# Performance work log

Measured on AMD Instinct MI355X. Metric: run time of the kernel, lower is better.

## Reference

```python
import jax, jax.numpy as jnp
import numpy as np

N, D = 768, 64
EPS = 1e-5

def _ln(x, g, b):
    u = x.mean(-1, keepdims=True)
    s = ((x - u) ** 2).mean(-1, keepdims=True)
    return g * (x - u) / jnp.sqrt(s + EPS) + b

def setup_inputs() -> dict:
    key = jax.random.key(0)
    ks = jax.random.split(key, 16)
    inp = {
        'corr_index': jax.random.normal(ks[0], (N, N, 2), dtype=jnp.float32),
        'nei_index': jax.random.randint(ks[1], (N, N), 0, 2, dtype=jnp.int32),
        'nei_num': jax.random.randint(ks[2], (N,), 0, N, dtype=jnp.int32),
        'hidden_state': jax.random.normal(ks[3], (N, D), dtype=jnp.float32),
        'cn': jax.random.normal(ks[4], (N, D), dtype=jnp.float32),
        # relativeLayer: MLP(2 -> D)
        'W_r': jax.random.normal(ks[5], (2, D)) * 0.01, 'b_r': jnp.zeros((D,)),
        'g_r': jnp.ones((D,)), 'be_r': jax.random.normal(ks[6], (D,)) * 0.02,
        # ngate: MLP_gate(3D -> D)
        'W_g': jax.random.normal(ks[7], (3 * D, D)) * 0.01, 'b_g': jnp.zeros((D,)),
        'g_g': jnp.ones((D,)), 'be_g': jax.random.normal(ks[8], (D,)) * 0.02,
        # WAr: MLP(3D -> 1)
        'W_a': jax.random.normal(ks[9], (3 * D, 1)) * 0.01, 'b_a': jnp.zeros((1,)),
        'g_a': jnp.ones((1,)), 'be_a': jnp.abs(jax.random.normal(ks[10], (1,))) * 0.02 + 0.01,
        # weight: MLP(D -> D)
        'W_w': jax.random.normal(ks[11], (D, D)) * 0.01, 'b_w': jnp.zeros((D,)),
        'g_w': jnp.ones((D,)), 'be_w': jax.random.normal(ks[12], (D,)) * 0.02,
    }
    return inp

def reference(corr_index, nei_index, nei_num, hidden_state, cn,
              W_r, b_r, g_r, be_r, W_g, b_g, g_g, be_g,
              W_a, b_a, g_a, be_a, W_w, b_w, g_w, be_w):
    n, d = hidden_state.shape
    mask = nei_index > 0  # [N,N]; (i,j): j is neighbor of i
    # relativeLayer on all pairs (values at masked positions match the torch gather)
    r = jax.nn.relu(_ln(corr_index @ W_r + b_r, g_r, be_r))  # [N,N,D]
    hi = jnp.broadcast_to(hidden_state[:, None, :], (n, n, d))  # hi_t: h[i]
    hj = jnp.broadcast_to(hidden_state[None, :, :], (n, n, d))  # nei_inputs: h[j]
    tmp = jnp.concatenate([r, hi, hj], axis=-1)  # [N,N,3D]
    nGate = jax.nn.sigmoid(_ln(tmp @ W_g + b_g, g_g, be_g))  # [N,N,D]
    tt = jax.nn.relu(_ln(tmp @ W_a + b_a, g_a, be_a))[..., 0]  # [N,N]
    Pos = jnp.where(mask, tt, 0.0)
    Pos = jnp.where(Pos == 0.0, -10000.0, Pos)  # Pos[Pos==0] = -10000
    Pos = jax.nn.softmax(Pos, axis=1)  # masked row-softmax over neighbors j
    # H[i,j] = h[j] * nGate[i,j] * Pos[i,j] at masked pairs, else 0
    H = jnp.where(mask[..., None], hj * nGate * Pos[..., None], 0.0)
    H_sum = jax.nn.relu(_ln(jnp.sum(H, axis=1) @ W_w + b_w, g_w, be_w))  # [N,D]
    C = H_sum + cn
    H_out = hidden_state + jnp.tanh(C)
    return (H_out, C)
```

## Files before the change

### kernel.cpp

```cpp
#include <hip/hip_runtime.h>


#define NN 768
#define DD 64
#define EPSF 1e-5f
#define LOG2E 1.44269504f

typedef __attribute__((ext_vector_type(8))) short short8;
typedef __attribute__((ext_vector_type(4))) float float4v;
typedef __attribute__((ext_vector_type(2))) float float2v;
typedef __attribute__((ext_vector_type(4))) unsigned short ushort4v;

__device__ __forceinline__ unsigned short f2bf(float f) {
  unsigned int u = __float_as_uint(f);
  u += 0x7fffu + ((u >> 16) & 1u);
  return (unsigned short)(u >> 16);
}

__device__ __forceinline__ float fast_tanh(float x) {
  float e = __builtin_amdgcn_exp2f(fminf(x, 20.f) * (2.f * LOG2E));
  return (e - 1.f) * __builtin_amdgcn_rcpf(e + 1.f);
}

__global__ __launch_bounds__(256) void prep_kernel(
    const float* __restrict__ hidden, const float* __restrict__ Wg,
    const float* __restrict__ bg, const float* __restrict__ Wr,
    const float* __restrict__ br, const float* __restrict__ gr,
    const float* __restrict__ ber, const float* __restrict__ gg,
    const float* __restrict__ beg, float* __restrict__ A_pre,
    float2v* __restrict__ BH, float4v* __restrict__ KT,
    float2v* __restrict__ GB, float* __restrict__ evec,
    unsigned short* __restrict__ WgT) {
  const int bid = blockIdx.x;
  const int tid = threadIdx.x;

  if (bid == NN / 4) {
    for (int idx = tid; idx < DD * DD; idx += 256) {
      int n = idx >> 6, k = idx & 63;
      WgT[idx] = f2bf(Wg[k * DD + n]);
    }
    if (tid < 64) {
      int t = tid;
      float w0 = Wr[t], w1 = Wr[DD + t], bb = br[t];
      float m0 = w0, m1 = w1, mb = bb;
      for (int m = 1; m < 64; m <<= 1) {
        m0 += __shfl_xor(m0, m);
        m1 += __shfl_xor(m1, m);
        mb += __shfl_xor(mb, m);
      }
      m0 *= (1.f / DD);
      m1 *= (1.f / DD);
      mb *= (1.f / DD);
      float a0 = w0 - m0, a1 = w1 - m1, ab = bb - mb;
      float grt = gr[t];
      float4v kt;
      kt[0] = grt * a0;
      kt[1] = grt * a1;
      kt[2] = grt * ab;
      kt[3] = ber[t];
      KT[t] = kt;
      float2v gb;
      gb[0] = -LOG2E * gg[t];
      gb[1] = -LOG2E * beg[t];
      GB[t] = gb;
      float e00 = a0 * a0, e11 = a1 * a1, ebb = ab * ab;
      float e01 = a0 * a1, e0b = a0 * ab, e1b = a1 * ab;
      for (int m = 1; m < 64; m <<= 1) {
        e00 += __shfl_xor(e00, m);
        e11 += __shfl_xor(e11, m);
        ebb += __shfl_xor(ebb, m);
        e01 += __shfl_xor(e01, m);
        e0b += __shfl_xor(e0b, m);
        e1b += __shfl_xor(e1b, m);
      }
      if (t == 0) {
        evec[0] = e00 * (1.f / DD);
        evec[1] = e11 * (1.f / DD);
        evec[2] = ebb * (1.f / DD);
        evec[3] = e01 * (1.f / DD);
        evec[4] = e0b * (1.f / DD);
        evec[5] = e1b * (1.f / DD);
      }
    }
    return;
  }

  const int w = tid >> 6;
  const int lane = tid & 63;
  const int i = bid * 4 + w;
  float hv = hidden[i * DD + lane];
  float a = bg[lane];
  float b = 0.f;
#pragma unroll 8
  for (int k = 0; k < DD; ++k) {
    float hk = __shfl(hv, k);
    a = fmaf(hk, Wg[(DD + k) * DD + lane], a);
    b = fmaf(hk, Wg[(2 * DD + k) * DD + lane], b);
  }
  A_pre[i * DD + lane] = a;
  float2v bh2;
  bh2[0] = b;
  bh2[1] = hv;
  BH[i * DD + lane] = bh2;
}

__global__ __launch_bounds__(512, 4) void gat_kernel(
    const int* __restrict__ nei, const float2v* __restrict__ corr2,
    const float* __restrict__ A_pre, const float2v* __restrict__ BH,
    const float4v* __restrict__ KT, const float2v* __restrict__ GB,
    const float* __restrict__ evec, const unsigned short* __restrict__ WgT,
    const float* __restrict__ hidden, const float* __restrict__ cn,
    const float* __restrict__ bea, const float* __restrict__ Ww,
    const float* __restrict__ bw, const float* __restrict__ gw,
    const float* __restrict__ bew, float* __restrict__ out) {
  __shared__ unsigned short Lst[NN + 16];
  __shared__ float2v CcL[NN + 16];
  __shared__ __align__(16) unsigned short Rt[8][16 * 72];
  __shared__ float red[8][DD];
  __shared__ int cLds;

  const int i = blockIdx.x;
  const int tid = threadIdx.x;
  const int wid = tid >> 6;
  const int lane = tid & 63;
  const int quad = lane >> 4;
  const int nl = lane & 15;

  if (tid == 0) cLds = 0;
  __syncthreads();
  {
    int jj = tid;
    if (nei[i * NN + jj] > 0) {
      int idx = atomicAdd(&cLds, 1);
      Lst[idx] = (unsigned short)jj;
      CcL[idx] = corr2[i * NN + jj];
    }
    jj = tid + 512;
    if (jj < NN && nei[i * NN + jj] > 0) {
      int idx = atomicAdd(&cLds, 1);
      Lst[idx] = (unsigned short)jj;
      CcL[idx] = corr2[i * NN + jj];
    }
  }
  __syncthreads();
  const int cnt = cLds;
  if (cnt > 0 && tid < 16) {
    Lst[cnt + tid] = Lst[0];
    CcL[cnt + tid] = CcL[0];
  }

  const float e00 = evec[0], e11 = evec[1], ebb = evec[2];
  const float e01 = evec[3], e0b = evec[4], e1b = evec[5];
  const float4v kt = KT[lane];

  short8 Bf[2][4];
#pragma unroll
  for (int ks = 0; ks < 2; ++ks)
#pragma unroll
    for (int nt = 0; nt < 4; ++nt)
      __builtin_memcpy(&Bf[ks][nt],
                       &WgT[(nt * 16 + nl) * DD + ks * 32 + quad * 8], 16);

  float ngg[4], nbeg[4], pre4[4];
#pragma unroll
  for (int nt = 0; nt < 4; ++nt) {
    int d = nt * 16 + nl;
    float2v gb = GB[d];
    ngg[nt] = gb[0];
    nbeg[nt] = gb[1];
    pre4[nt] = A_pre[i * DD + d];
  }

  float accT[4] = {0.f, 0.f, 0.f, 0.f};
  __syncthreads();

  for (int base = wid * 16; base < cnt; base += 128) {
    ushort4v l4;
    __builtin_memcpy(&l4, &Lst[base + quad * 4], 8);
    float2v cc = CcL[base + nl];
    float2v bh[4][4];
#pragma unroll
    for (int rr = 0; rr < 4; ++rr) {
      const int jpr = (int)l4[rr];
#pragma unroll
      for (int nt = 0; nt < 4; ++nt) bh[rr][nt] = BH[jpr * DD + nt * 16 + nl];
    }
    asm volatile("" ::: "memory");

    float var = cc[0] * cc[0] * e00 + cc[1] * cc[1] * e11 + ebb +
                2.f * (cc[0] * cc[1] * e01 + cc[0] * e0b + cc[1] * e1b);
    float iv = __builtin_amdgcn_rsqf(var + EPSF);

#pragma unroll
    for (int q = 0; q < 16; ++q) {
      float sc0 = __shfl(cc[0], q);
      float sc1 = __shfl(cc[1], q);
      float siv = __shfl(iv, q);
      float s3 = fmaf(sc0, kt[0], fmaf(sc1, kt[1], kt[2]));
      float r = fmaxf(0.f, fmaf(siv, s3, kt[3]));
      Rt[wid][q * 72 + lane] = f2bf(r);
    }

    short8 a0, a1;
    __builtin_memcpy(&a0, &Rt[wid][nl * 72 + quad * 8], 16);
    __builtin_memcpy(&a1, &Rt[wid][nl * 72 + 32 + quad * 8], 16);
    float4v acc[4];
#pragma unroll
    for (int nt = 0; nt < 4; ++nt) {
      float4v z = {0.f, 0.f, 0.f, 0.f};
      z = __builtin_amdgcn_mfma_f32_16x16x32_bf16(a0, Bf[0][nt], z, 0, 0, 0);
      z = __builtin_amdgcn_mfma_f32_16x16x32_bf16(a1, Bf[1][nt], z, 0, 0, 0);
      acc[nt] = z;
    }

#pragma unroll
    for (int rr = 0; rr < 4; ++rr) {
      const float pvr = (base + quad * 4 + rr < cnt) ? 1.f : 0.f;
      float y0 = acc[0][rr] + pre4[0] + bh[rr][0][0];
      float y1 = acc[1][rr] + pre4[1] + bh[rr][1][0];
      float y2 = acc[2][rr] + pre4[2] + bh[rr][2][0];
      float y3 = acc[3][rr] + pre4[3] + bh[rr][3][0];
      float s = y0 + y1 + y2 + y3;
      float qq = y0 * y0 + y1 * y1 + y2 * y2 + y3 * y3;
#pragma unroll
      for (int m = 1; m < 16; m <<= 1) {
        s += __shfl_xor(s, m);
        qq += __shfl_xor(qq, m);
      }
      float u = s * (1.f / DD);
      float vv = qq * (1.f / DD) - u * u;
      float inv = __builtin_amdgcn_rsqf(vv + EPSF);
      float g0 = __builtin_amdgcn_exp2f(fmaf(ngg[0] * (y0 - u), inv, nbeg[0]));
      float g1 = __builtin_amdgcn_exp2f(fmaf(ngg[1] * (y1 - u), inv, nbeg[1]));
      float g2 = __builtin_amdgcn_exp2f(fmaf(ngg[2] * (y2 - u), inv, nbeg[2]));
      float g3 = __builtin_amdgcn_exp2f(fmaf(ngg[3] * (y3 - u), inv, nbeg[3]));
      accT[0] =
          fmaf(__builtin_amdgcn_rcpf(1.f + g0) * pvr, bh[rr][0][1], accT[0]);
      accT[1] =
          fmaf(__builtin_amdgcn_rcpf(1.f + g1) * pvr, bh[rr][1][1], accT[1]);
      accT[2] =
          fmaf(__builtin_amdgcn_rcpf(1.f + g2) * pvr, bh[rr][2][1], accT[2]);
      accT[3] =
          fmaf(__builtin_amdgcn_rcpf(1.f + g3) * pvr, bh[rr][3][1], accT[3]);
    }
  }

#pragma unroll
  for (int nt = 0; nt < 4; ++nt) {
    accT[nt] += __shfl_xor(accT[nt], 16);
    accT[nt] += __shfl_xor(accT[nt], 32);
  }
  if (lane < 16) {
#pragma unroll
    for (int nt = 0; nt < 4; ++nt) red[wid][nt * 16 + nl] = accT[nt];
  }
  __syncthreads();

  if (tid < 64) {
    const int d = tid;
    float hs = 0.f;
#pragma unroll
    for (int w = 0; w < 8; ++w) hs += red[w][d];
    float tta = fmaxf(bea[0], 0.f);
    float wgt = (tta > 0.f && cnt > 0) ? __builtin_amdgcn_rcpf((float)cnt)
                                       : (1.f / (float)NN);
    hs *= wgt;

    float dotv = bw[d];
#pragma unroll 8
    for (int k = 0; k < DD; ++k) {
      float hk = __shfl(hs, k);
      dotv = fmaf(hk, Ww[k * DD + d], dotv);
    }
    float s = dotv, qq = dotv * dotv;
#pragma unroll
    for (int m = 1; m < 64; m <<= 1) {
      s += __shfl_xor(s, m);
      qq += __shfl_xor(qq, m);
    }
    float u = s * (1.f / DD);
    float var2 = qq * (1.f / DD) - u * u;
    float inv = __builtin_amdgcn_rsqf(var2 + EPSF);
    float val = fmaxf(0.f, fmaf(gw[d], (dotv - u) * inv, bew[d]));
    float Cv = val + cn[i * DD + d];
    out[i * DD + d] = hidden[i * DD + d] + fast_tanh(Cv);
    out[NN * DD + i * DD + d] = Cv;
  }
}

extern "C" void kernel_launch(void* const* d_in, const int* in_sizes, int n_in,
                              void* d_out, int out_size, void* d_ws,
                              size_t ws_size, hipStream_t stream) {
  const float* corr = (const float*)d_in[0];
  const int* nei = (const int*)d_in[1];
  const float* hidden = (const float*)d_in[3];
  const float* cn = (const float*)d_in[4];
  const float* Wr = (const float*)d_in[5];
  const float* br = (const float*)d_in[6];
  const float* gr = (const float*)d_in[7];
  const float* ber = (const float*)d_in[8];
  const float* Wg = (const float*)d_in[9];
  const float* bg = (const float*)d_in[10];
  const float* gg = (const float*)d_in[11];
  const float* beg = (const float*)d_in[12];
  const float* bea = (const float*)d_in[16];
  const float* Ww = (const float*)d_in[17];
  const float* bw = (const float*)d_in[18];
  const float* gw = (const float*)d_in[19];
  const float* bew = (const float*)d_in[20];
  float* out = (float*)d_out;

  float* ws = (float*)d_ws;
  float* A_pre = ws;
  float2v* BH = (float2v*)(ws + 49152);
  float4v* KT = (float4v*)(ws + 147456);
  float2v* GB = (float2v*)(ws + 147712);
  float* evec = ws + 147840;
  unsigned short* WgT = (unsigned short*)(ws + 147856);

  prep_kernel<<<NN / 4 + 1, 256, 0, stream>>>(hidden, Wg, bg, Wr, br, gr, ber,
                                              gg, beg, A_pre, BH, KT, GB, evec,
                                              WgT);
  gat_kernel<<<NN, 512, 0, stream>>>((const int*)nei, (const float2v*)corr,
                                     A_pre, BH, KT, GB, evec, WgT, hidden, cn,
                                     bea, Ww, bw, gw, bew, out);
}
```

Measured before the change: 129.3 us.

## Split prep GEMV across waves, hoist gat setup loads, prefetch next neighbor batch

The prep kernel now uses one block per row, with four waves each covering a quarter of the K dimension and a shared-memory reduction, instead of one wave per row over all 64 K. This raises parallelism from 193 to 769 blocks. In the main kernel, the constant loads (evec, KT, WgT fragments, GB, A_pre) move ahead of the neighbor-compaction phase so their latency overlaps it. Each wave also prefetches the next iteration's neighbor indices and coordinates from LDS while computing the current batch. This costs extra registers and an extra block sync in prep.

Result: slower. 132.6 us (+2.6%).

```diff
diff --git a/kernel.cpp b/kernel.cpp
--- a/kernel.cpp
+++ b/kernel.cpp
@@ -34,7 +34,7 @@
   const int bid = blockIdx.x;
   const int tid = threadIdx.x;
 
-  if (bid == NN / 4) {
+  if (bid == NN) {
     for (int idx = tid; idx < DD * DD; idx += 256) {
       int n = idx >> 6, k = idx & 63;
       WgT[idx] = f2bf(Wg[k * DD + n]);
@@ -85,23 +85,33 @@
     return;
   }
 
+  __shared__ float redA[4][DD];
+  __shared__ float redB[4][DD];
   const int w = tid >> 6;
   const int lane = tid & 63;
-  const int i = bid * 4 + w;
+  const int i = bid;
   float hv = hidden[i * DD + lane];
-  float a = bg[lane];
-  float b = 0.f;
-#pragma unroll 8
-  for (int k = 0; k < DD; ++k) {
+  float a = 0.f, b = 0.f;
+#pragma unroll
+  for (int j = 0; j < 16; ++j) {
+    int k = w * 16 + j;
     float hk = __shfl(hv, k);
     a = fmaf(hk, Wg[(DD + k) * DD + lane], a);
     b = fmaf(hk, Wg[(2 * DD + k) * DD + lane], b);
   }
-  A_pre[i * DD + lane] = a;
-  float2v bh2;
-  bh2[0] = b;
-  bh2[1] = hv;
-  BH[i * DD + lane] = bh2;
+  redA[w][lane] = a;
+  redB[w][lane] = b;
+  __syncthreads();
+  if (tid < 64) {
+    float aa = bg[lane] + redA[0][lane] + redA[1][lane] + redA[2][lane] +
+               redA[3][lane];
+    float bb = redB[0][lane] + redB[1][lane] + redB[2][lane] + redB[3][lane];
+    A_pre[i * DD + lane] = aa;
+    float2v bh2;
+    bh2[0] = bb;
+    bh2[1] = hv;
+    BH[i * DD + lane] = bh2;
+  }
 }
 
 __global__ __launch_bounds__(512, 4) void gat_kernel(
@@ -126,6 +136,26 @@
   const int quad = lane >> 4;
   const int nl = lane & 15;
 
+  const float e00 = evec[0], e11 = evec[1], ebb = evec[2];
+  const float e01 = evec[3], e0b = evec[4], e1b = evec[5];
+  const float4v kt = KT[lane];
+  short8 Bf[2][4];
+#pragma unroll
+  for (int ks = 0; ks < 2; ++ks)
+#pragma unroll
+    for (int nt = 0; nt < 4; ++nt)
+      __builtin_memcpy(&Bf[ks][nt],
+                       &WgT[(nt * 16 + nl) * DD + ks * 32 + quad * 8], 16);
+  float ngg[4], nbeg[4], pre4[4];
+#pragma unroll
+  for (int nt = 0; nt < 4; ++nt) {
+    int d = nt * 16 + nl;
+    float2v gb = GB[d];
+    ngg[nt] = gb[0];
+    nbeg[nt] = gb[1];
+    pre4[nt] = A_pre[i * DD + d];
+  }
+
   if (tid == 0) cLds = 0;
   __syncthreads();
   {
@@ -149,35 +179,25 @@
     CcL[cnt + tid] = CcL[0];
   }
 
-  const float e00 = evec[0], e11 = evec[1], ebb = evec[2];
-  const float e01 = evec[3], e0b = evec[4], e1b = evec[5];
-  const float4v kt = KT[lane];
-
-  short8 Bf[2][4];
-#pragma unroll
-  for (int ks = 0; ks < 2; ++ks)
-#pragma unroll
-    for (int nt = 0; nt < 4; ++nt)
-      __builtin_memcpy(&Bf[ks][nt],
-                       &WgT[(nt * 16 + nl) * DD + ks * 32 + quad * 8], 16);
-
-  float ngg[4], nbeg[4], pre4[4];
-#pragma unroll
-  for (int nt = 0; nt < 4; ++nt) {
-    int d = nt * 16 + nl;
-    float2v gb = GB[d];
-    ngg[nt] = gb[0];
-    nbeg[nt] = gb[1];
-    pre4[nt] = A_pre[i * DD + d];
-  }
-
   float accT[4] = {0.f, 0.f, 0.f, 0.f};
   __syncthreads();
 
+  ushort4v l4 = {0, 0, 0, 0};
+  float2v cc = {0.f, 0.f};
+  if (wid * 16 < cnt) {
+    __builtin_memcpy(&l4, &Lst[wid * 16 + quad * 4], 8);
+    cc = CcL[wid * 16 + nl];
+  }
+
   for (int base = wid * 16; base < cnt; base += 128) {
-    ushort4v l4;
-    __builtin_memcpy(&l4, &Lst[base + quad * 4], 8);
-    float2v cc = CcL[base + nl];
+    const int nb = base + 128;
+    ushort4v l4n = l4;
+    float2v ccn = cc;
+    if (nb < cnt) {
+      __builtin_memcpy(&l4n, &Lst[nb + quad * 4], 8);
+      ccn = CcL[nb + nl];
+    }
+
     float2v bh[4][4];
 #pragma unroll
     for (int rr = 0; rr < 4; ++rr) {
@@ -243,6 +263,9 @@
       accT[3] =
           fmaf(__builtin_amdgcn_rcpf(1.f + g3) * pvr, bh[rr][3][1], accT[3]);
     }
+
+    l4 = l4n;
+    cc = ccn;
   }
 
 #pragma unroll
@@ -318,9 +341,8 @@
   float* evec = ws + 147840;
   unsigned short* WgT = (unsigned short*)(ws + 147856);
 
-  prep_kernel<<<NN / 4 + 1, 256, 0, stream>>>(hidden, Wg, bg, Wr, br, gr, ber,
-                                              gg, beg, A_pre, BH, KT, GB, evec,
-                                              WgT);
+  prep_kernel<<<NN + 1, 256, 0, stream>>>(hidden, Wg, bg, Wr, br, gr, ber, gg,
+                                          beg, A_pre, BH, KT, GB, evec, WgT);
   gat_kernel<<<NN, 512, 0, stream>>>((const int*)nei, (const float2v*)corr,
                                      A_pre, BH, KT, GB, evec, WgT, hidden, cn,
                                      bea, Ww, bw, gw, bew, out);
```
